# Kernel tuning notes

Hardware: AMD Instinct MI355X
Metric: run time of the kernel (lower is better)

The kernel has to match this reference:

```python
import jax, jax.numpy as jnp
import numpy as np

# static config (matches init_kwargs)
T_K = 3      # Time_kernel
K = 3        # spatial_kernel_side_length
C = 64       # dim_hidden
H = 4        # num_head
D = 16       # dim_head
NL = 2       # num_layers
F = 3        # dim_feature
N, S1, S2 = 32, 32, 32
P = K // 2
L1 = T_K // 2
M = T_K * K * K
EPS = 1e-5


def _neighbor_mask():
    # spatial_neighbor_mask with an all-ones city mask: offset (k1,k2) is a valid
    # neighbor of cell (s1,s2) iff it lands inside the grid.
    m = np.zeros((S1, S2, K, K), dtype=bool)
    s1 = np.arange(S1); s2 = np.arange(S2)
    for k1 in range(K):
        v1 = (s1 + k1 - P >= 0) & (s1 + k1 - P < S1)
        for k2 in range(K):
            v2 = (s2 + k2 - P >= 0) & (s2 + k2 - P < S2)
            m[:, :, k1, k2] = v1[:, None] & v2[None, :]
    mf = m.reshape(S1, S2, K * K)
    # tiled across Time_kernel, flattened in (t, k1, k2) order like the torch code
    return np.tile(mf[:, :, None, :], (1, 1, T_K, 1)).reshape(S1, S2, M)

_MASK = jnp.asarray(_neighbor_mask())


def _forward(x, W_in, b_in, W_out, b_out, Wq, bq, Wk, bk, Wv, bv):
    # BatchNorm2d (training-mode batch stats, affine = identity init)
    mean = x.mean(axis=(0, 1, 2))
    var = ((x - mean) ** 2).mean(axis=(0, 1, 2))
    h = (x - mean) * jax.lax.rsqrt(var + EPS)
    h = h @ W_in + b_in  # [N,S1,S2,C]

    for l in range(NL):
        res = h  # res_block_thickness = 1 -> residual every layer
        q = (h @ Wq[l] + bq[l]).reshape(N, S1, S2, H, D)
        # spatial unfold (nn.Unfold, padding=K//2, stride=1)
        hp = jnp.pad(h, ((0, 0), (P, P), (P, P), (0, 0)))
        u = jnp.stack([jnp.stack([hp[:, k1:k1 + S1, k2:k2 + S2, :]
                                  for k2 in range(K)]) for k1 in range(K)])  # [K,K,N,S1,S2,C]
        # time unfold (zero-padded shifts along N)
        up = jnp.pad(u, ((0, 0), (0, 0), (L1, L1), (0, 0), (0, 0), (0, 0)))
        ut = jnp.stack([up[:, :, t:t + N] for t in range(T_K)])  # [T,K,K,N,S1,S2,C]
        # per-offset single-Linear MLPs (kernel_neurons=[C,C]), batched over T,K,K
        ks = jnp.einsum('tijnabc,tijcd->nabtijd', ut, Wk[l]) + bk[l]
        vs = jnp.einsum('tijnabc,tijcd->nabtijd', ut, Wv[l]) + bv[l]
        kM = ks.reshape(N, S1, S2, M, H, D)
        vM = vs.reshape(N, S1, S2, M, H, D)
        # unscaled dot-product attention over valid neighbors (masked == dropped)
        sc = jnp.einsum('nabmhd,nabhd->nabhm', kM, q)
        sc = jnp.where(_MASK[None, :, :, None, :], sc, -1e30)
        w = jax.nn.softmax(sc, axis=-1)
        h = jnp.einsum('nabhm,nabmhd->nabhd', w, vM).reshape(N, S1, S2, C)
        h = h + res

    return h @ W_out + b_out  # [N,S1,S2,F]


def setup_inputs() -> dict:
    key = jax.random.key(0)
    k = jax.random.split(key, 11)
    s = 0.05
    return {
        'x': jax.random.normal(k[0], (N, S1, S2, F), jnp.float32),
        'W_in': jax.random.normal(k[1], (F, C), jnp.float32) * s,
        'b_in': jax.random.normal(k[2], (C,), jnp.float32) * s,
        'W_out': jax.random.normal(k[3], (C, F), jnp.float32) * s,
        'b_out': jax.random.normal(k[4], (F,), jnp.float32) * s,
        'Wq': jax.random.normal(k[5], (NL, C, C), jnp.float32) * s,
        'bq': jax.random.normal(k[6], (NL, C), jnp.float32) * s,
        'Wk': jax.random.normal(k[7], (NL, T_K, K, K, C, C), jnp.float32) * s,
        'bk': jax.random.normal(k[8], (NL, T_K, K, K, C), jnp.float32) * s,
        'Wv': jax.random.normal(k[9], (NL, T_K, K, K, C, C), jnp.float32) * s,
        'bv': jax.random.normal(k[10], (NL, T_K, K, K, C), jnp.float32) * s,
    }


def reference(x, W_in, b_in, W_out, b_out, Wq, bq, Wk, bk, Wv, bv):
    return _forward(x, W_in, b_in, W_out, b_out, Wq, bq, Wk, bk, Wv, bv)
```

## Files before the change

### kernel.cpp

```cpp
#include <hip/hip_runtime.h>
#include <hip/hip_bf16.h>


typedef short short8_t __attribute__((ext_vector_type(8)));
typedef float floatx4 __attribute__((ext_vector_type(4)));

__device__ __forceinline__ short f2bs(float f) {
    __hip_bfloat16 h = __float2bfloat16(f);
    return *reinterpret_cast<short*>(&h);
}
__device__ __forceinline__ int hn_idx(int rowid, int chunk) {
    return rowid * 64 + ((chunk ^ (rowid & 7)) << 3);
}

__global__ void prep_kernel(const float* __restrict__ Wq, const float* __restrict__ Wk,
                            const float* __restrict__ Wv, short* __restrict__ dst,
                            const float* __restrict__ x, float* __restrict__ sums) {
    if (blockIdx.x < 220) {
        int t = blockIdx.x * 256 + threadIdx.x;
        if (t >= 110 * 512) return;
        int mat  = t >> 9;
        int rem  = t & 511;
        int kk   = rem >> 8;
        int nt   = (rem >> 6) & 3;
        int lane = rem & 63;
        int krow = kk * 32 + (lane >> 4) * 8;
        int col  = nt * 16 + (lane & 15);
        const float* W;
        if (mat < 2)       W = Wq + mat * 4096;
        else if (mat < 56) W = Wk + (mat - 2) * 4096;
        else               W = Wv + (mat - 56) * 4096;
        short8_t v;
        #pragma unroll
        for (int j = 0; j < 8; ++j) v[j] = f2bs(W[(krow + j) * 64 + col]);
        *(short8_t*)&dst[(size_t)mat * 4096 + ((kk * 4 + nt) * 64 + lane) * 8] = v;
    } else {
        int bid = blockIdx.x - 220;
        int t = bid * 256 + threadIdx.x;
        const float4* x4 = (const float4*)x;
        float4 v0 = x4[t * 3 + 0], v1 = x4[t * 3 + 1], v2 = x4[t * 3 + 2];
        float vv[6];
        vv[0] = v0.x + v0.w + v1.z + v2.y;
        vv[1] = v0.y + v1.x + v1.w + v2.z;
        vv[2] = v0.z + v1.y + v2.x + v2.w;
        vv[3] = v0.x*v0.x + v0.w*v0.w + v1.z*v1.z + v2.y*v2.y;
        vv[4] = v0.y*v0.y + v1.x*v1.x + v1.w*v1.w + v2.z*v2.z;
        vv[5] = v0.z*v0.z + v1.y*v1.y + v2.x*v2.x + v2.w*v2.w;
        #pragma unroll
        for (int i = 0; i < 6; ++i) {
            #pragma unroll
            for (int off = 1; off < 64; off <<= 1) vv[i] += __shfl_xor(vv[i], off);
        }
        __shared__ float part[4][6];
        if ((threadIdx.x & 63) == 0) {
            #pragma unroll
            for (int i = 0; i < 6; ++i) part[threadIdx.x >> 6][i] = vv[i];
        }
        __syncthreads();
        if (threadIdx.x < 6)
            sums[bid * 8 + threadIdx.x] = part[0][threadIdx.x] + part[1][threadIdx.x] +
                                          part[2][threadIdx.x] + part[3][threadIdx.x];
    }
}

template <bool FIRST>
__global__ __launch_bounds__(512, 4)
void layer_fused(const float* __restrict__ x, const float* __restrict__ sums,
                 const float* __restrict__ W_in, const float* __restrict__ b_in,
                 const float* __restrict__ hres, const short* __restrict__ hbf,
                 float* __restrict__ hout, short* __restrict__ hbfout,
                 const float* __restrict__ Wout, const float* __restrict__ bout,
                 float* __restrict__ out,
                 const short* __restrict__ wqB, const float* __restrict__ bq,
                 const short* __restrict__ wkB, const float* __restrict__ bk,
                 const short* __restrict__ wvB, const float* __restrict__ bv) {
    __shared__ short HnS[324 * 64];
    __shared__ float Waux[256];
    __shared__ float bn6[6];

    const int tid = threadIdx.x;
    const int bb0 = blockIdx.x * 4, a = blockIdx.y, nb = blockIdx.z;

    if (FIRST) {
        if (tid < 3) {
            float s = 0.f, qq = 0.f;
            #pragma unroll
            for (int p = 0; p < 32; ++p) { s += sums[p * 8 + tid]; qq += sums[p * 8 + 3 + tid]; }
            float mean = s * (1.f / 32768.f);
            float var  = qq * (1.f / 32768.f) - mean * mean;
            bn6[tid]     = mean;
            bn6[3 + tid] = rsqrtf(var + 1e-5f);
        }
        if (tid < 192)      Waux[tid] = W_in[tid];
        else if (tid < 256) Waux[tid] = b_in[tid - 192];
    } else {
        if (tid < 192)      Waux[tid] = Wout[tid];
        else if (tid < 195) Waux[tid] = bout[tid - 192];
    }
    __syncthreads();

    float mean0, mean1, mean2, rs0, rs1, rs2;
    if (FIRST) {
        mean0 = bn6[0]; mean1 = bn6[1]; mean2 = bn6[2];
        rs0 = bn6[3]; rs1 = bn6[4]; rs2 = bn6[5];
    }

    for (int id = tid; id < 2592; id += 512) {
        int rowid = id >> 3, cc = id & 7;
        int r = rowid % 18;
        int rw = rowid / 18;
        int spa = rw / 6, jcol = rw - spa * 6;
        int aa = a + spa - 1, bb = bb0 + jcol - 1;
        int n  = nb * 16 + r - 1;
        short8_t v = {0, 0, 0, 0, 0, 0, 0, 0};
        if ((unsigned)n < 32u && (unsigned)aa < 32u && (unsigned)bb < 32u) {
            int cell = (n * 32 + aa) * 32 + bb;
            if (FIRST) {
                float xn0 = (x[cell*3+0] - mean0) * rs0;
                float xn1 = (x[cell*3+1] - mean1) * rs1;
                float xn2 = (x[cell*3+2] - mean2) * rs2;
                #pragma unroll
                for (int j = 0; j < 8; ++j) {
                    int c = cc * 8 + j;
                    float h = Waux[192+c] + xn0*Waux[c] + xn1*Waux[64+c] + xn2*Waux[128+c];
                    v[j] = f2bs(h);
                }
            } else {
                v = *(const short8_t*)&hbf[cell * 64 + cc * 8];
            }
        }
        *(short8_t*)&HnS[hn_idx(rowid, cc)] = v;
    }
    __syncthreads();

    const int lane = tid & 63;
    const int wv8  = tid >> 6;
    const int w    = wv8 & 3;
    const int g2   = wv8 >> 2;
    const int e    = lane & 15;
    const int q    = lane >> 4;
    const int c0   = w * 16 + q * 4;

    bool va[3], vb[6];
    #pragma unroll
    for (int d = 0; d < 3; ++d) va[d] = (unsigned)(a + d - 1) < 32u;
    #pragma unroll
    for (int j = 0; j < 6; ++j) vb[j] = (unsigned)(bb0 + j - 1) < 32u;

    floatx4 qv[4];
    {
        short8_t wq0 = *(const short8_t*)&wqB[((0 * 4 + w) * 64 + lane) * 8];
        short8_t wq1 = *(const short8_t*)&wqB[((1 * 4 + w) * 64 + lane) * 8];
        const float4 bq4 = *(const float4*)&bq[c0];
        #pragma unroll
        for (int ci = 0; ci < 4; ++ci) {
            const int row = (6 + ci + 1) * 18 + e + 1;
            short8_t h0 = *(const short8_t*)&HnS[hn_idx(row, q)];
            short8_t h1 = *(const short8_t*)&HnS[hn_idx(row, 4 + q)];
            floatx4 acc = {0, 0, 0, 0};
            acc = __builtin_amdgcn_mfma_f32_16x16x32_bf16(wq0, h0, acc, 0, 0, 0);
            acc = __builtin_amdgcn_mfma_f32_16x16x32_bf16(wq1, h1, acc, 0, 0, 0);
            qv[ci][0] = acc[0] + bq4.x; qv[ci][1] = acc[1] + bq4.y;
            qv[ci][2] = acc[2] + bq4.z; qv[ci][3] = acc[3] + bq4.w;
        }
    }

    floatx4 o[4] = {{0,0,0,0},{0,0,0,0},{0,0,0,0},{0,0,0,0}};
    float mx[4] = {-1e30f, -1e30f, -1e30f, -1e30f};
    float ss[4] = {0.f, 0.f, 0.f, 0.f};

    const int mstart = g2 ? 14 : 0;
    const int mend   = g2 ? 27 : 14;
    for (int m = mstart; m < mend; ++m) {
        const int t  = m / 9;
        const int sp = m - t * 9;
        const int di = sp / 3, dj = sp - di * 3;
        if (!va[di]) continue;
        short8_t wk0 = *(const short8_t*)&wkB[m * 4096 + ((0 * 4 + w) * 64 + lane) * 8];
        short8_t wk1 = *(const short8_t*)&wkB[m * 4096 + ((1 * 4 + w) * 64 + lane) * 8];
        short8_t wv0 = *(const short8_t*)&wvB[m * 4096 + ((0 * 4 + w) * 64 + lane) * 8];
        short8_t wv1 = *(const short8_t*)&wvB[m * 4096 + ((1 * 4 + w) * 64 + lane) * 8];
        const float4 bk4 = *(const float4*)&bk[m * 64 + c0];
        const float4 bv4 = *(const float4*)&bv[m * 64 + c0];
        const int rowb = (di * 6 + dj) * 18 + e + t;
        #pragma unroll
        for (int ci = 0; ci < 4; ++ci) {
            if (!vb[dj + ci]) continue;
            const int row = rowb + ci * 18;
            short8_t h0 = *(const short8_t*)&HnS[hn_idx(row, q)];
            short8_t h1 = *(const short8_t*)&HnS[hn_idx(row, 4 + q)];
            floatx4 kacc = {0, 0, 0, 0};
            kacc = __builtin_amdgcn_mfma_f32_16x16x32_bf16(wk0, h0, kacc, 0, 0, 0);
            kacc = __builtin_amdgcn_mfma_f32_16x16x32_bf16(wk1, h1, kacc, 0, 0, 0);
            floatx4 vacc = {0, 0, 0, 0};
            vacc = __builtin_amdgcn_mfma_f32_16x16x32_bf16(wv0, h0, vacc, 0, 0, 0);
            vacc = __builtin_amdgcn_mfma_f32_16x16x32_bf16(wv1, h1, vacc, 0, 0, 0);
            float p = (kacc[0] + bk4.x) * qv[ci][0] + (kacc[1] + bk4.y) * qv[ci][1]
                    + (kacc[2] + bk4.z) * qv[ci][2] + (kacc[3] + bk4.w) * qv[ci][3];
            p += __shfl_xor(p, 16);
            p += __shfl_xor(p, 32);
            float mnew  = fmaxf(mx[ci], p);
            float scale = __expf(mx[ci] - mnew);
            float wgt   = __expf(p - mnew);
            ss[ci] = ss[ci] * scale + wgt;
            mx[ci] = mnew;
            o[ci][0] = o[ci][0] * scale + wgt * (vacc[0] + bv4.x);
            o[ci][1] = o[ci][1] * scale + wgt * (vacc[1] + bv4.y);
            o[ci][2] = o[ci][2] * scale + wgt * (vacc[2] + bv4.z);
            o[ci][3] = o[ci][3] * scale + wgt * (vacc[3] + bv4.w);
        }
    }

    __syncthreads();
    float* stbuf = (float*)HnS;
    if (g2 == 1) {
        #pragma unroll
        for (int ci = 0; ci < 4; ++ci) {
            float* d = &stbuf[(((w * 64 + lane) * 4) + ci) * 6];
            d[0] = mx[ci]; d[1] = ss[ci];
            d[2] = o[ci][0]; d[3] = o[ci][1]; d[4] = o[ci][2]; d[5] = o[ci][3];
        }
    }
    __syncthreads();
    if (g2 == 0) {
        #pragma unroll
        for (int ci = 0; ci < 4; ++ci) {
            const float* d = &stbuf[(((w * 64 + lane) * 4) + ci) * 6];
            float m1 = d[0], s1 = d[1];
            float M  = fmaxf(mx[ci], m1);
            float e0 = __expf(mx[ci] - M);
            float e1 = __expf(m1 - M);
            float inv = 1.0f / (ss[ci] * e0 + s1 * e1);
            o[ci][0] = (o[ci][0] * e0 + d[2] * e1) * inv;
            o[ci][1] = (o[ci][1] * e0 + d[3] * e1) * inv;
            o[ci][2] = (o[ci][2] * e0 + d[4] * e1) * inv;
            o[ci][3] = (o[ci][3] * e0 + d[5] * e1) * inv;
        }
    }

    const int n = nb * 16 + e;
    if (FIRST) {
        if (g2 == 0) {
            #pragma unroll
            for (int ci = 0; ci < 4; ++ci) {
                int cell = (n * 32 + a) * 32 + bb0 + ci;
                float xn0 = (x[cell*3+0] - mean0) * rs0;
                float xn1 = (x[cell*3+1] - mean1) * rs1;
                float xn2 = (x[cell*3+2] - mean2) * rs2;
                float4 hv; float* hvp = (float*)&hv;
                short4 hb; short* hbp = (short*)&hb;
                #pragma unroll
                for (int i = 0; i < 4; ++i) {
                    int c = c0 + i;
                    float res = Waux[192+c] + xn0*Waux[c] + xn1*Waux[64+c] + xn2*Waux[128+c];
                    float v = o[ci][i] + res;
                    hvp[i] = v;
                    hbp[i] = f2bs(v);
                }
                *(float4*)&hout[cell * 64 + c0] = hv;
                *(short4*)&hbfout[cell * 64 + c0] = hb;
            }
        }
    } else {
        __syncthreads();
        float* hf = (float*)HnS;
        if (g2 == 0) {
            #pragma unroll
            for (int ci = 0; ci < 4; ++ci) {
                float4 res = *(const float4*)&hres[((n * 32 + a) * 32 + bb0 + ci) * 64 + c0];
                float* d = &hf[(ci * 16 + e) * 68 + c0];
                d[0] = o[ci][0] + res.x;
                d[1] = o[ci][1] + res.y;
                d[2] = o[ci][2] + res.z;
                d[3] = o[ci][3] + res.w;
            }
        }
        __syncthreads();
        if (tid < 192) {
            int rowglob = tid / 3, f = tid - rowglob * 3;
            int ci = rowglob >> 4, row = rowglob & 15;
            float acc = Waux[192 + f];
            #pragma unroll 8
            for (int cc = 0; cc < 64; ++cc) acc += hf[rowglob * 68 + cc] * Waux[cc * 3 + f];
            int nn = nb * 16 + row;
            out[((nn * 32 + a) * 32 + bb0 + ci) * 3 + f] = acc;
        }
    }
}

extern "C" void kernel_launch(void* const* d_in, const int* in_sizes, int n_in,
                              void* d_out, int out_size, void* d_ws, size_t ws_size,
                              hipStream_t stream) {
    const float* x     = (const float*)d_in[0];
    const float* W_in  = (const float*)d_in[1];
    const float* b_in  = (const float*)d_in[2];
    const float* W_out = (const float*)d_in[3];
    const float* b_out = (const float*)d_in[4];
    const float* Wq    = (const float*)d_in[5];
    const float* bq    = (const float*)d_in[6];
    const float* Wk    = (const float*)d_in[7];
    const float* bk    = (const float*)d_in[8];
    const float* Wv    = (const float*)d_in[9];
    const float* bv    = (const float*)d_in[10];

    float* ws    = (float*)d_ws;
    float* sums  = ws;
    float* h1    = ws + 256;
    short* h1bf  = (short*)(h1 + 2097152);
    short* wB    = h1bf + 2097152;

    prep_kernel<<<252, 256, 0, stream>>>(Wq, Wk, Wv, wB, x, sums);

    const short* wq0 = wB;                const short* wq1 = wB + 4096;
    const short* wk0 = wB + 2 * 4096;     const short* wk1 = wB + (2 + 27) * 4096;
    const short* wv0 = wB + 56 * 4096;    const short* wv1 = wB + (56 + 27) * 4096;

    dim3 grid(8, 32, 2);
    layer_fused<true><<<grid, 512, 0, stream>>>(
        x, sums, W_in, b_in, nullptr, nullptr, h1, h1bf,
        nullptr, nullptr, nullptr,
        wq0, bq, wk0, bk, wv0, bv);
    layer_fused<false><<<grid, 512, 0, stream>>>(
        nullptr, nullptr, nullptr, nullptr, h1, h1bf, nullptr, nullptr,
        W_out, b_out, (float*)d_out,
        wq1, bq + 64, wk1, bk + 1728, wv1, bv + 1728);
}
```

Before: 160.9 us.

## Fuse prep and both layers into one persistent kernel with grid barriers

Merges the weight-conversion/BN-stats prep kernel and both layer kernels into a single 512-block launch that synchronises through atomic-counter grid barriers, removing the inter-kernel launch gaps. It also drops the online-softmax max tracking in favour of plain exp sums, stores only the bf16 hidden state and reads the residual back from bf16, and replaces the divisions with multiply-shift index math. Risks: the grid barrier deadlocks if all 512 blocks are not co-resident. Skipping the max subtraction can overflow for large logits, and using a bf16 residual lowers accuracy.

```diff
diff --git a/kernel.cpp b/kernel.cpp
--- a/kernel.cpp
+++ b/kernel.cpp
@@ -9,83 +9,46 @@
     __hip_bfloat16 h = __float2bfloat16(f);
     return *reinterpret_cast<short*>(&h);
 }
+__device__ __forceinline__ float bs2f(short s) {
+    union { unsigned u; float f; } v;
+    v.u = ((unsigned)(unsigned short)s) << 16;
+    return v.f;
+}
 __device__ __forceinline__ int hn_idx(int rowid, int chunk) {
     return rowid * 64 + ((chunk ^ (rowid & 7)) << 3);
 }
 
-__global__ void prep_kernel(const float* __restrict__ Wq, const float* __restrict__ Wk,
-                            const float* __restrict__ Wv, short* __restrict__ dst,
-                            const float* __restrict__ x, float* __restrict__ sums) {
-    if (blockIdx.x < 220) {
-        int t = blockIdx.x * 256 + threadIdx.x;
-        if (t >= 110 * 512) return;
-        int mat  = t >> 9;
-        int rem  = t & 511;
-        int kk   = rem >> 8;
-        int nt   = (rem >> 6) & 3;
-        int lane = rem & 63;
-        int krow = kk * 32 + (lane >> 4) * 8;
-        int col  = nt * 16 + (lane & 15);
-        const float* W;
-        if (mat < 2)       W = Wq + mat * 4096;
-        else if (mat < 56) W = Wk + (mat - 2) * 4096;
-        else               W = Wv + (mat - 56) * 4096;
-        short8_t v;
-        #pragma unroll
-        for (int j = 0; j < 8; ++j) v[j] = f2bs(W[(krow + j) * 64 + col]);
-        *(short8_t*)&dst[(size_t)mat * 4096 + ((kk * 4 + nt) * 64 + lane) * 8] = v;
-    } else {
-        int bid = blockIdx.x - 220;
-        int t = bid * 256 + threadIdx.x;
-        const float4* x4 = (const float4*)x;
-        float4 v0 = x4[t * 3 + 0], v1 = x4[t * 3 + 1], v2 = x4[t * 3 + 2];
-        float vv[6];
-        vv[0] = v0.x + v0.w + v1.z + v2.y;
-        vv[1] = v0.y + v1.x + v1.w + v2.z;
-        vv[2] = v0.z + v1.y + v2.x + v2.w;
-        vv[3] = v0.x*v0.x + v0.w*v0.w + v1.z*v1.z + v2.y*v2.y;
-        vv[4] = v0.y*v0.y + v1.x*v1.x + v1.w*v1.w + v2.z*v2.z;
-        vv[5] = v0.z*v0.z + v1.y*v1.y + v2.x*v2.x + v2.w*v2.w;
-        #pragma unroll
-        for (int i = 0; i < 6; ++i) {
-            #pragma unroll
-            for (int off = 1; off < 64; off <<= 1) vv[i] += __shfl_xor(vv[i], off);
-        }
-        __shared__ float part[4][6];
-        if ((threadIdx.x & 63) == 0) {
-            #pragma unroll
-            for (int i = 0; i < 6; ++i) part[threadIdx.x >> 6][i] = vv[i];
-        }
-        __syncthreads();
-        if (threadIdx.x < 6)
-            sums[bid * 8 + threadIdx.x] = part[0][threadIdx.x] + part[1][threadIdx.x] +
-                                          part[2][threadIdx.x] + part[3][threadIdx.x];
-    }
+__device__ __forceinline__ void grid_bar(int* cnt, int target, int tid) {
+    __syncthreads();
+    if (tid == 0) {
+        __threadfence();
+        __hip_atomic_fetch_add(cnt, 1, __ATOMIC_ACQ_REL, __HIP_MEMORY_SCOPE_AGENT);
+        while (__hip_atomic_load(cnt, __ATOMIC_ACQUIRE, __HIP_MEMORY_SCOPE_AGENT) < target)
+            __builtin_amdgcn_s_sleep(8);
+    }
+    __syncthreads();
 }
 
 template <bool FIRST>
-__global__ __launch_bounds__(512, 4)
-void layer_fused(const float* __restrict__ x, const float* __restrict__ sums,
-                 const float* __restrict__ W_in, const float* __restrict__ b_in,
-                 const float* __restrict__ hres, const short* __restrict__ hbf,
-                 float* __restrict__ hout, short* __restrict__ hbfout,
-                 const float* __restrict__ Wout, const float* __restrict__ bout,
-                 float* __restrict__ out,
-                 const short* __restrict__ wqB, const float* __restrict__ bq,
-                 const short* __restrict__ wkB, const float* __restrict__ bk,
-                 const short* __restrict__ wvB, const float* __restrict__ bv) {
-    __shared__ short HnS[324 * 64];
-    __shared__ float Waux[256];
-    __shared__ float bn6[6];
-
-    const int tid = threadIdx.x;
-    const int bb0 = blockIdx.x * 4, a = blockIdx.y, nb = blockIdx.z;
+__device__ __forceinline__ void layer_body(
+        short* HnS, float* Waux, float* bn6, int bid, int tid,
+        const float* __restrict__ x, const float* __restrict__ sums,
+        const float* __restrict__ W_in, const float* __restrict__ b_in,
+        const short* __restrict__ hbf_in, short* __restrict__ hbf_out,
+        const float* __restrict__ Wout, const float* __restrict__ bout,
+        float* __restrict__ out,
+        const short* __restrict__ wqB, const float* __restrict__ bq,
+        const short* __restrict__ wkB, const float* __restrict__ bk,
+        const short* __restrict__ wvB, const float* __restrict__ bv) {
+    const int bb0 = (bid & 7) * 4;
+    const int a   = (bid >> 3) & 31;
+    const int nb  = bid >> 8;
 
     if (FIRST) {
         if (tid < 3) {
             float s = 0.f, qq = 0.f;
             #pragma unroll
-            for (int p = 0; p < 32; ++p) { s += sums[p * 8 + tid]; qq += sums[p * 8 + 3 + tid]; }
+            for (int p = 0; p < 16; ++p) { s += sums[p * 8 + tid]; qq += sums[p * 8 + 3 + tid]; }
             float mean = s * (1.f / 32768.f);
             float var  = qq * (1.f / 32768.f) - mean * mean;
             bn6[tid]     = mean;
@@ -99,7 +62,7 @@
     }
     __syncthreads();
 
-    float mean0, mean1, mean2, rs0, rs1, rs2;
+    float mean0 = 0, mean1 = 0, mean2 = 0, rs0 = 0, rs1 = 0, rs2 = 0;
     if (FIRST) {
         mean0 = bn6[0]; mean1 = bn6[1]; mean2 = bn6[2];
         rs0 = bn6[3]; rs1 = bn6[4]; rs2 = bn6[5];
@@ -126,7 +89,7 @@
                     v[j] = f2bs(h);
                 }
             } else {
-                v = *(const short8_t*)&hbf[cell * 64 + cc * 8];
+                v = *(const short8_t*)&hbf_in[cell * 64 + cc * 8];
             }
         }
         *(short8_t*)&HnS[hn_idx(rowid, cc)] = v;
@@ -166,15 +129,15 @@
     }
 
     floatx4 o[4] = {{0,0,0,0},{0,0,0,0},{0,0,0,0},{0,0,0,0}};
-    float mx[4] = {-1e30f, -1e30f, -1e30f, -1e30f};
     float ss[4] = {0.f, 0.f, 0.f, 0.f};
 
     const int mstart = g2 ? 14 : 0;
     const int mend   = g2 ? 27 : 14;
     for (int m = mstart; m < mend; ++m) {
-        const int t  = m / 9;
-        const int sp = m - t * 9;
-        const int di = sp / 3, dj = sp - di * 3;
+        const int t  = (m * 57) >> 9;
+        const int sp = m - 9 * t;
+        const int di = (sp * 11) >> 5;
+        const int dj = sp - 3 * di;
         if (!va[di]) continue;
         short8_t wk0 = *(const short8_t*)&wkB[m * 4096 + ((0 * 4 + w) * 64 + lane) * 8];
         short8_t wk1 = *(const short8_t*)&wkB[m * 4096 + ((1 * 4 + w) * 64 + lane) * 8];
@@ -199,15 +162,12 @@
                     + (kacc[2] + bk4.z) * qv[ci][2] + (kacc[3] + bk4.w) * qv[ci][3];
             p += __shfl_xor(p, 16);
             p += __shfl_xor(p, 32);
-            float mnew  = fmaxf(mx[ci], p);
-            float scale = __expf(mx[ci] - mnew);
-            float wgt   = __expf(p - mnew);
-            ss[ci] = ss[ci] * scale + wgt;
-            mx[ci] = mnew;
-            o[ci][0] = o[ci][0] * scale + wgt * (vacc[0] + bv4.x);
-            o[ci][1] = o[ci][1] * scale + wgt * (vacc[1] + bv4.y);
-            o[ci][2] = o[ci][2] * scale + wgt * (vacc[2] + bv4.z);
-            o[ci][3] = o[ci][3] * scale + wgt * (vacc[3] + bv4.w);
+            float wgt = __expf(p);
+            ss[ci] += wgt;
+            o[ci][0] += wgt * (vacc[0] + bv4.x);
+            o[ci][1] += wgt * (vacc[1] + bv4.y);
+            o[ci][2] += wgt * (vacc[2] + bv4.z);
+            o[ci][3] += wgt * (vacc[3] + bv4.w);
         }
     }
 
@@ -216,25 +176,21 @@
     if (g2 == 1) {
         #pragma unroll
         for (int ci = 0; ci < 4; ++ci) {
-            float* d = &stbuf[(((w * 64 + lane) * 4) + ci) * 6];
-            d[0] = mx[ci]; d[1] = ss[ci];
-            d[2] = o[ci][0]; d[3] = o[ci][1]; d[4] = o[ci][2]; d[5] = o[ci][3];
+            float* d = &stbuf[(((w * 64 + lane) * 4) + ci) * 5];
+            d[0] = ss[ci];
+            d[1] = o[ci][0]; d[2] = o[ci][1]; d[3] = o[ci][2]; d[4] = o[ci][3];
         }
     }
     __syncthreads();
     if (g2 == 0) {
         #pragma unroll
         for (int ci = 0; ci < 4; ++ci) {
-            const float* d = &stbuf[(((w * 64 + lane) * 4) + ci) * 6];
-            float m1 = d[0], s1 = d[1];
-            float M  = fmaxf(mx[ci], m1);
-            float e0 = __expf(mx[ci] - M);
-            float e1 = __expf(m1 - M);
-            float inv = 1.0f / (ss[ci] * e0 + s1 * e1);
-            o[ci][0] = (o[ci][0] * e0 + d[2] * e1) * inv;
-            o[ci][1] = (o[ci][1] * e0 + d[3] * e1) * inv;
-            o[ci][2] = (o[ci][2] * e0 + d[4] * e1) * inv;
-            o[ci][3] = (o[ci][3] * e0 + d[5] * e1) * inv;
+            const float* d = &stbuf[(((w * 64 + lane) * 4) + ci) * 5];
+            float inv = 1.0f / (ss[ci] + d[0]);
+            o[ci][0] = (o[ci][0] + d[1]) * inv;
+            o[ci][1] = (o[ci][1] + d[2]) * inv;
+            o[ci][2] = (o[ci][2] + d[3]) * inv;
+            o[ci][3] = (o[ci][3] + d[4]) * inv;
         }
     }
 
@@ -247,18 +203,14 @@
                 float xn0 = (x[cell*3+0] - mean0) * rs0;
                 float xn1 = (x[cell*3+1] - mean1) * rs1;
                 float xn2 = (x[cell*3+2] - mean2) * rs2;
-                float4 hv; float* hvp = (float*)&hv;
                 short4 hb; short* hbp = (short*)&hb;
                 #pragma unroll
                 for (int i = 0; i < 4; ++i) {
                     int c = c0 + i;
                     float res = Waux[192+c] + xn0*Waux[c] + xn1*Waux[64+c] + xn2*Waux[128+c];
-                    float v = o[ci][i] + res;
-                    hvp[i] = v;
-                    hbp[i] = f2bs(v);
+                    hbp[i] = f2bs(o[ci][i] + res);
                 }
-                *(float4*)&hout[cell * 64 + c0] = hv;
-                *(short4*)&hbfout[cell * 64 + c0] = hb;
+                *(short4*)&hbf_out[cell * 64 + c0] = hb;
             }
         }
     } else {
@@ -267,12 +219,13 @@
         if (g2 == 0) {
             #pragma unroll
             for (int ci = 0; ci < 4; ++ci) {
-                float4 res = *(const float4*)&hres[((n * 32 + a) * 32 + bb0 + ci) * 64 + c0];
+                int cell = (n * 32 + a) * 32 + bb0 + ci;
+                short4 hb = *(const short4*)&hbf_in[cell * 64 + c0];
                 float* d = &hf[(ci * 16 + e) * 68 + c0];
-                d[0] = o[ci][0] + res.x;
-                d[1] = o[ci][1] + res.y;
-                d[2] = o[ci][2] + res.z;
-                d[3] = o[ci][3] + res.w;
+                d[0] = o[ci][0] + bs2f(hb.x);
+                d[1] = o[ci][1] + bs2f(hb.y);
+                d[2] = o[ci][2] + bs2f(hb.z);
+                d[3] = o[ci][3] + bs2f(hb.w);
             }
         }
         __syncthreads();
@@ -286,6 +239,88 @@
             out[((nn * 32 + a) * 32 + bb0 + ci) * 3 + f] = acc;
         }
     }
+}
+
+__global__ __launch_bounds__(512, 4)
+void fused_all(const float* __restrict__ x,
+               const float* __restrict__ W_in, const float* __restrict__ b_in,
+               const float* __restrict__ W_out, const float* __restrict__ b_out,
+               const float* __restrict__ Wq, const float* __restrict__ bq,
+               const float* __restrict__ Wk, const float* __restrict__ bk,
+               const float* __restrict__ Wv, const float* __restrict__ bv,
+               int* __restrict__ cnt, float* __restrict__ sums,
+               short* __restrict__ h1bf, short* __restrict__ wB,
+               float* __restrict__ out) {
+    __shared__ short HnS[324 * 64];
+    __shared__ float Waux[256];
+    __shared__ float bn6[6];
+
+    const int tid = threadIdx.x;
+    const int bid = blockIdx.x;
+
+    if (bid < 110) {
+        int gid = bid * 512 + tid;
+        int mat  = gid >> 9;
+        int rem  = gid & 511;
+        int kk   = rem >> 8;
+        int nt   = (rem >> 6) & 3;
+        int lane = rem & 63;
+        int krow = kk * 32 + (lane >> 4) * 8;
+        int col  = nt * 16 + (lane & 15);
+        const float* W;
+        if (mat < 2)       W = Wq + mat * 4096;
+        else if (mat < 56) W = Wk + (mat - 2) * 4096;
+        else               W = Wv + (mat - 56) * 4096;
+        short8_t v;
+        #pragma unroll
+        for (int j = 0; j < 8; ++j) v[j] = f2bs(W[(krow + j) * 64 + col]);
+        *(short8_t*)&wB[(size_t)mat * 4096 + ((kk * 4 + nt) * 64 + lane) * 8] = v;
+    } else if (bid < 126) {
+        int bid2 = bid - 110;
+        int t = bid2 * 512 + tid;
+        const float4* x4 = (const float4*)x;
+        float4 v0 = x4[t * 3 + 0], v1 = x4[t * 3 + 1], v2 = x4[t * 3 + 2];
+        float vv[6];
+        vv[0] = v0.x + v0.w + v1.z + v2.y;
+        vv[1] = v0.y + v1.x + v1.w + v2.z;
+        vv[2] = v0.z + v1.y + v2.x + v2.w;
+        vv[3] = v0.x*v0.x + v0.w*v0.w + v1.z*v1.z + v2.y*v2.y;
+        vv[4] = v0.y*v0.y + v1.x*v1.x + v1.w*v1.w + v2.z*v2.z;
+        vv[5] = v0.z*v0.z + v1.y*v1.y + v2.x*v2.x + v2.w*v2.w;
+        #pragma unroll
+        for (int i = 0; i < 6; ++i) {
+            #pragma unroll
+            for (int off = 1; off < 64; off <<= 1) vv[i] += __shfl_xor(vv[i], off);
+        }
+        __shared__ float part[8][6];
+        if ((tid & 63) == 0) {
+            #pragma unroll
+            for (int i = 0; i < 6; ++i) part[tid >> 6][i] = vv[i];
+        }
+        __syncthreads();
+        if (tid < 6) {
+            float acc = 0.f;
+            #pragma unroll
+            for (int p = 0; p < 8; ++p) acc += part[p][tid];
+            sums[bid2 * 8 + tid] = acc;
+        }
+    }
+
+    grid_bar(cnt, 512, tid);
+
+    const short* wq0 = wB;                const short* wq1 = wB + 4096;
+    const short* wk0 = wB + 2 * 4096;     const short* wk1 = wB + (2 + 27) * 4096;
+    const short* wv0 = wB + 56 * 4096;    const short* wv1 = wB + (56 + 27) * 4096;
+
+    layer_body<true>(HnS, Waux, bn6, bid, tid, x, sums, W_in, b_in,
+                     nullptr, h1bf, nullptr, nullptr, nullptr,
+                     wq0, bq, wk0, bk, wv0, bv);
+
+    grid_bar(cnt, 1024, tid);
+
+    layer_body<false>(HnS, Waux, bn6, bid, tid, x, sums, nullptr, nullptr,
+                      h1bf, nullptr, W_out, b_out, out,
+                      wq1, bq + 64, wk1, bk + 1728, wv1, bv + 1728);
 }
 
 extern "C" void kernel_launch(void* const* d_in, const int* in_sizes, int n_in,
@@ -304,24 +339,15 @@
     const float* bv    = (const float*)d_in[10];
 
     float* ws    = (float*)d_ws;
-    float* sums  = ws;
-    float* h1    = ws + 256;
-    short* h1bf  = (short*)(h1 + 2097152);
+    int*   cnt   = (int*)ws;
+    float* sums  = ws + 64;
+    short* h1bf  = (short*)(ws + 256);
     short* wB    = h1bf + 2097152;
-
-    prep_kernel<<<252, 256, 0, stream>>>(Wq, Wk, Wv, wB, x, sums);
-
-    const short* wq0 = wB;                const short* wq1 = wB + 4096;
-    const short* wk0 = wB + 2 * 4096;     const short* wk1 = wB + (2 + 27) * 4096;
-    const short* wv0 = wB + 56 * 4096;    const short* wv1 = wB + (56 + 27) * 4096;
-
-    dim3 grid(8, 32, 2);
-    layer_fused<true><<<grid, 512, 0, stream>>>(
-        x, sums, W_in, b_in, nullptr, nullptr, h1, h1bf,
-        nullptr, nullptr, nullptr,
-        wq0, bq, wk0, bk, wv0, bv);
-    layer_fused<false><<<grid, 512, 0, stream>>>(
-        nullptr, nullptr, nullptr, nullptr, h1, h1bf, nullptr, nullptr,
-        W_out, b_out, (float*)d_out,
-        wq1, bq + 64, wk1, bk + 1728, wv1, bv + 1728);
-}
+    float* out   = (float*)d_out;
+
+    hipMemsetAsync(cnt, 0, 256, stream);
+
+    fused_all<<<512, 512, 0, stream>>>(x, W_in, b_in, W_out, b_out,
+                                       Wq, bq, Wk, bk, Wv, bv,
+                                       cnt, sums, h1bf, wB, out);
+}
```

After: 276.6 us. 1.72x slower.
